# Kernel tuning notes

Hardware: AMD Instinct MI355X
Metric: run time of the kernel (lower is better)

## Reference

```python
import jax, jax.numpy as jnp
import numpy as np

B, T, H = 256, 512, 1024


def setup_inputs() -> dict:
    key = jax.random.key(0)
    ks = jax.random.split(key, 11)
    s = 1.0 / np.sqrt(H)
    u = lambda k, shape: jax.random.uniform(k, shape, jnp.float32, -s, s)
    return {
        "x": jax.random.normal(ks[0], (B, T), jnp.float32),
        "W_ih1": u(ks[1], (4 * H, 1)),
        "W_hh1": u(ks[2], (4 * H, H)),
        "b_ih1": u(ks[3], (4 * H,)),
        "b_hh1": u(ks[4], (4 * H,)),
        "W_ih2": u(ks[5], (4 * H, H)),
        "W_hh2": u(ks[6], (4 * H, H)),
        "b_ih2": u(ks[7], (4 * H,)),
        "b_hh2": u(ks[8], (4 * H,)),
        "W_out": u(ks[9], (1, H)),
        "b_out": u(ks[10], (1,)),
        "future": 0,
    }


def _lstm_cell(x, h, c, W_ih, W_hh, b):
    # PyTorch LSTMCell gate order: i, f, g, o
    gates = x @ W_ih.T + h @ W_hh.T + b
    i, f, g, o = jnp.split(gates, 4, axis=-1)
    c_new = jax.nn.sigmoid(f) * c + jax.nn.sigmoid(i) * jnp.tanh(g)
    h_new = jax.nn.sigmoid(o) * jnp.tanh(c_new)
    return h_new, c_new


def reference(x, W_ih1, W_hh1, b_ih1, b_hh1, W_ih2, W_hh2, b_ih2, b_hh2, W_out, b_out, future):
    Bn = x.shape[0]
    Hd = W_hh1.shape[1]
    b1 = b_ih1 + b_hh1
    b2 = b_ih2 + b_hh2

    def step(carry, x_t):
        h1, c1, h2, c2 = carry
        h1, c1 = _lstm_cell(x_t, h1, c1, W_ih1, W_hh1, b1)
        h2, c2 = _lstm_cell(h1, h2, c2, W_ih2, W_hh2, b2)
        out = h2 @ W_out.T + b_out  # [B, 1]
        return (h1, c1, h2, c2), out

    xs = x.T[:, :, None]  # [T, B, 1]
    carry0 = tuple(jnp.zeros((Bn, Hd), x.dtype) for _ in range(4))
    carry, outs = jax.lax.scan(step, carry0, xs)  # outs: [T, B, 1]
    outputs = [outs[:, :, 0].T]  # [B, T]

    # closed-loop future prediction (future is a static Python int)
    out = outs[-1]
    for _ in range(future):
        carry, out = step(carry, out)
        outputs.append(out)
    return jnp.concatenate(outputs, axis=1)
```

## Files before the change

kernel.cpp:

```cpp
#include <hip/hip_runtime.h>
#include <hip/hip_cooperative_groups.h>
#include <math.h>

namespace cg = cooperative_groups;

#define Bsz 256
#define Tsz 512
#define GSTR 258

using half8 = __attribute__((ext_vector_type(8))) _Float16;
using half4 = __attribute__((ext_vector_type(4))) _Float16;
using f32x4 = __attribute__((ext_vector_type(4))) float;

#define MFMA_V(acc, a, b) (acc) = __builtin_amdgcn_mfma_f32_16x16x32_f16((a), (b), (acc), 0, 0, 0)
#define INV2048 (1.0f / 2048.0f)

__device__ __forceinline__ float sigm(float v)   { return 1.0f / (1.0f + expf(-v)); }
__device__ __forceinline__ float tanh_f(float v) { float e = expf(2.0f * v); return 1.0f - 2.0f / (e + 1.0f); }

__device__ __forceinline__ void split8(const float* p, half8& hi, half8& lo) {
    float4 v0 = *(const float4*)p, v1 = *(const float4*)(p + 4);
    float vv[8] = {v0.x, v0.y, v0.z, v0.w, v1.x, v1.y, v1.z, v1.w};
    #pragma unroll
    for (int j = 0; j < 8; ++j) {
        hi[j] = (_Float16)vv[j];
        lo[j] = (_Float16)((vv[j] - (float)hi[j]) * 2048.0f);
    }
}

__device__ __forceinline__ void st_h4(_Float16* p, half4 v) {
    unsigned long long u;
    __builtin_memcpy(&u, &v, 8);
    __hip_atomic_store((unsigned long long*)(void*)p, u,
                       __ATOMIC_RELAXED, __HIP_MEMORY_SCOPE_AGENT);
}
__device__ __forceinline__ void st_f(float* p, float v) {
    __hip_atomic_store(p, v, __ATOMIC_RELAXED, __HIP_MEMORY_SCOPE_AGENT);
}

__device__ __forceinline__ unsigned ag_add(unsigned* p, unsigned v) {
    return __hip_atomic_fetch_add(p, v, __ATOMIC_RELAXED, __HIP_MEMORY_SCOPE_AGENT);
}
__device__ __forceinline__ unsigned ag_ld(unsigned* p) {
    return __hip_atomic_load(p, __ATOMIC_RELAXED, __HIP_MEMORY_SCOPE_AGENT);
}

__device__ __forceinline__ void busy_fma(float& z) {
    #pragma unroll
    for (int i = 0; i < 16; ++i)
        z = __builtin_fmaf(z, 1.0000001f, 1e-9f);
    asm volatile("" :: "v"(z));
}

__device__ __forceinline__ void step_barrier(unsigned* arrX, unsigned* flagX,
                                             unsigned* bar1, unsigned* dummyv,
                                             unsigned* relFlag,
                                             int isLead, unsigned xcc,
                                             unsigned nLead, unsigned nBlkX,
                                             unsigned it1) {
    __syncthreads();
    if ((threadIdx.x >> 6) == 0) {
        if ((threadIdx.x & 63) == 0) {
            float z = 1.0f;
            ag_add(&arrX[xcc << 5], 1u);
            if (isLead) {
                while (ag_ld(&arrX[xcc << 5]) < nBlkX * it1) busy_fma(z);
                ag_add(bar1, 1u);
                while (ag_ld(bar1) < nLead * it1) busy_fma(z);
                if ((it1 & 3u) == 0u)
                    __hip_atomic_fetch_add(&dummyv[xcc << 5], 1u,
                                           __ATOMIC_ACQ_REL, __HIP_MEMORY_SCOPE_AGENT);
                ag_add(&flagX[xcc << 5], 1u);
            } else {
                while (ag_ld(&flagX[xcc << 5]) < it1) busy_fma(z);
            }
            asm volatile("s_waitcnt vmcnt(0)" ::: "memory");
            __hip_atomic_store(relFlag, it1, __ATOMIC_RELAXED,
                               __HIP_MEMORY_SCOPE_WORKGROUP);
        }
        asm volatile("buffer_inv sc0" ::: "memory");
    } else {
        float z = 1.0f + (float)(threadIdx.x & 63) * 1e-8f;
        while (__hip_atomic_load(relFlag, __ATOMIC_RELAXED,
                                 __HIP_MEMORY_SCOPE_WORKGROUP) < it1)
            busy_fma(z);
        asm volatile("buffer_inv sc0" ::: "memory");
    }
}

__global__ __launch_bounds__(512, 1) void lstm_persist(
    const float* __restrict__ x,
    const float* __restrict__ W_ih1, const float* __restrict__ W_hh1,
    const float* __restrict__ b_ih1, const float* __restrict__ b_hh1,
    const float* __restrict__ W_ih2, const float* __restrict__ W_hh2,
    const float* __restrict__ b_ih2, const float* __restrict__ b_hh2,
    const float* __restrict__ W_out, const float* __restrict__ b_out,
    float* __restrict__ out, char* __restrict__ ws)
{
    __shared__ float gAcc[32 * GSTR];
    __shared__ float poArr[2 * GSTR];
    __shared__ float bp[32], wihp[32], woutp[8];
    __shared__ float bouts_s;
    __shared__ unsigned isLead_s, xcc_s, nLead_s, nBlkX_s;
    __shared__ unsigned relFlag_s;

    cg::grid_group grid = cg::this_grid();

    const int tid  = threadIdx.x;
    const int lane = tid & 63;
    const int wv   = tid >> 6;
    const int m    = lane & 15;
    const int quad = lane >> 4;
    const int bx   = blockIdx.x;
    const bool isL2 = (bx >= 128);
    const int rg   = isL2 ? (bx - 128) : bx;
    const int HO   = rg << 3;

    float*    xT       = (float*)ws;
    _Float16* hswz     = (_Float16*)(ws + (512 << 10));
    float*    partials = (float*)(ws + (512 << 10) + (8 << 20));
    unsigned* bar0     = (unsigned*)(ws + (512 << 10) + (8 << 20) + (512 << 10));
    unsigned* arrX     = bar0 + 512;
    unsigned* flagX    = bar0 + 768;
    unsigned* bar1     = bar0 + 1024;
    unsigned* nLeadCt  = bar0 + 1057;
    unsigned* claimA   = bar0 + 1088;
    unsigned* dummyv   = bar0 + 1536;

    #define HBUF(p, l, hl) (hswz + ((((p) << 2) | ((l) << 1) | (hl)) << 18))

    if (bx == 0)
        for (int i = tid; i < 2048; i += 512) bar0[i] = 0u;
    if (tid < 32) {
        const int row = ((tid & 3) << 10) + HO + (tid >> 2);
        if (!isL2) {
            bp[tid]   = b_ih1[row] + b_hh1[row];
            wihp[tid] = W_ih1[row];
        } else {
            bp[tid] = b_ih2[row] + b_hh2[row];
            if (tid < 8) woutp[tid] = W_out[HO + tid];
        }
        if (tid == 0) { bouts_s = b_out[0]; relFlag_s = 0u; }
    }
    {
        const int gidx = bx * 512 + tid;
        *(float4*)((char*)hswz + (6u << 20) + (size_t)gidx * 16) = make_float4(0, 0, 0, 0);
        xT[gidx] = x[(gidx & 255) * Tsz + (gidx >> 8)];
    }

    grid.sync();

    if (tid == 0) {
        unsigned xcc;
        asm volatile("s_getreg_b32 %0, hwreg(HW_REG_XCC_ID)" : "=s"(xcc));
        xcc &= 7u;
        xcc_s = xcc;
        unsigned old = ag_add(&claimA[xcc << 5], 1u);
        isLead_s = (old == 0u);
        if (old == 0u)
            ag_add(nLeadCt, 1u);
    }
    grid.sync();
    if (tid == 0) {
        nLead_s = ag_ld(nLeadCt);
        nBlkX_s = ag_ld(&claimA[xcc_s << 5]);
    }
    __syncthreads();
    const int      isLead = (int)isLead_s;
    const unsigned xcc    = xcc_s;
    const unsigned nLead  = nLead_s;
    const unsigned nBlkX  = nBlkX_s;

    const int b_ep = tid & 255, hg = tid >> 8;
    const int k0e  = HO + (hg << 2);
    const int wofs = ((b_ep >> 4) << 14) + ((k0e >> 5) << 9)
                   + (((b_ep & 15) | (((k0e >> 3) & 3) << 4)) << 3) + (k0e & 7);

    if (!isL2) {
        half8 wh[2][4], wl[2][4];
        #pragma unroll
        for (int mt = 0; mt < 2; ++mt) {
            const int pr = (mt << 4) + m;
            const size_t rw = (size_t)(((pr & 3) << 10) + HO + (pr >> 2)) << 10;
            #pragma unroll
            for (int kt = 0; kt < 4; ++kt) {
                const int k = (wv << 7) + (kt << 5) + (quad << 3);
                split8(W_hh1 + rw + k, wh[mt][kt], wl[mt][kt]);
            }
        }
        for (int idx = tid; idx < 8192; idx += 512) {
            const int p = idx >> 8, b = idx & 255;
            gAcc[p * GSTR + b] = bp[p] + xT[b] * wihp[p];
        }
        __syncthreads();
        float cr[4] = {0, 0, 0, 0};

        for (int it = 0; it <= Tsz; ++it) {
            const int sW = it & 3;
            const int sR = (it + 3) & 3;
            const int sP = it & 3;

            float xnext = 0.0f;
            if (it + 1 < Tsz) xnext = xT[((it + 1) << 8) + b_ep];

            if (wv == 0 && it >= 2) {
                const float* pp = partials + (sP << 15) + (bx << 7);
                float s = pp[lane] + pp[lane + 64];
                s += __shfl_xor(s, 32); s += __shfl_xor(s, 16); s += __shfl_xor(s, 8);
                s += __shfl_xor(s, 4);  s += __shfl_xor(s, 2);  s += __shfl_xor(s, 1);
                if (lane == 0) st_f(&out[(bx << 9) + (it - 2)], bouts_s + s);
            }

            if (it < Tsz) {
                const _Float16* bhB = HBUF(sR, 0, 0);
                const _Float16* blB = HBUF(sR, 0, 1);
                const int lo_off = (wv << 11) + (lane << 3);
                #pragma unroll 2
                for (int bi = 0; bi < 16; ++bi) {
                    const int btl = (bi + (wv << 1)) & 15;
                    const _Float16* ph = bhB + (btl << 14) + lo_off;
                    const _Float16* pl = blB + (btl << 14) + lo_off;
                    half8 bh[4], bl[4];
                    #pragma unroll
                    for (int kt = 0; kt < 4; ++kt) {
                        bh[kt] = *(const half8*)(ph + (kt << 9));
                        bl[kt] = *(const half8*)(pl + (kt << 9));
                    }
                    f32x4 a0[2] = {(f32x4){0,0,0,0}, (f32x4){0,0,0,0}};
                    f32x4 a1[2] = {(f32x4){0,0,0,0}, (f32x4){0,0,0,0}};
                    #pragma unroll
                    for (int kt = 0; kt < 4; ++kt) {
                        MFMA_V(a0[0], wh[0][kt], bh[kt]);
                        MFMA_V(a1[0], wh[0][kt], bl[kt]);
                        MFMA_V(a1[0], wl[0][kt], bh[kt]);
                        MFMA_V(a0[1], wh[1][kt], bh[kt]);
                        MFMA_V(a1[1], wh[1][kt], bl[kt]);
                        MFMA_V(a1[1], wl[1][kt], bh[kt]);
                    }
                    const int col = (btl << 4) + m;
                    #pragma unroll
                    for (int mt = 0; mt < 2; ++mt)
                        #pragma unroll
                        for (int r = 0; r < 4; ++r)
                            atomicAdd(&gAcc[((mt << 4) + (quad << 2) + r) * GSTR + col],
                                      a0[mt][r] + a1[mt][r] * INV2048);
                }
            }

            __syncthreads();

            if (it < Tsz) {
                half4 hhi, hlo;
                #pragma unroll
                for (int j = 0; j < 4; ++j) {
                    const int p = (hg << 4) + (j << 2);
                    const float gi = gAcc[(p + 0) * GSTR + b_ep];
                    const float gf = gAcc[(p + 1) * GSTR + b_ep];
                    const float gg = gAcc[(p + 2) * GSTR + b_ep];
                    const float go = gAcc[(p + 3) * GSTR + b_ep];
                    const float c  = sigm(gf) * cr[j] + sigm(gi) * tanh_f(gg);
                    cr[j] = c;
                    const float hn = sigm(go) * tanh_f(c);
                    hhi[j] = (_Float16)hn;
                    hlo[j] = (_Float16)((hn - (float)hhi[j]) * 2048.0f);
                }
                st_h4(HBUF(sW, 0, 0) + wofs, hhi);
                st_h4(HBUF(sW, 0, 1) + wofs, hlo);
                if (it + 1 < Tsz) {
                    #pragma unroll
                    for (int p = (hg << 4); p < (hg << 4) + 16; ++p)
                        gAcc[p * GSTR + b_ep] = bp[p] + xnext * wihp[p];
                }
            }

            step_barrier(arrX, flagX, bar1, dummyv, &relFlag_s,
                         isLead, xcc, nLead, nBlkX, (unsigned)(it + 1));
        }
    } else {
        half8 wh[2][8], wl[2][8];
        #pragma unroll
        for (int mt = 0; mt < 2; ++mt) {
            const int pr = (mt << 4) + m;
            const size_t rw = (size_t)(((pr & 3) << 10) + HO + (pr >> 2)) << 10;
            #pragma unroll
            for (int kt = 0; kt < 8; ++kt) {
                const int k = (wv << 8) + (kt << 5) + (quad << 3);
                const float* p = (k < 1024) ? (W_ih2 + rw + k)
                                            : (W_hh2 + rw + k - 1024);
                split8(p, wh[mt][kt], wl[mt][kt]);
            }
        }
        for (int idx = tid; idx < 8192; idx += 512) {
            const int p = idx >> 8, b = idx & 255;
            gAcc[p * GSTR + b] = bp[p];
        }
        __syncthreads();
        float cr[4] = {0, 0, 0, 0};

        for (int it = 0; it <= Tsz; ++it) {
            const int sR1 = (it + 3) & 3;
            const int sW2 = (it + 3) & 3;
            const int sR2 = (it + 2) & 3;
            const int sP  = it & 3;
            const int sPW = (it + 1) & 3;

            if (wv == 0 && it >= 2) {
                const float* pp = partials + (sP << 15) + (bx << 7);
                float s = pp[lane] + pp[lane + 64];
                s += __shfl_xor(s, 32); s += __shfl_xor(s, 16); s += __shfl_xor(s, 8);
                s += __shfl_xor(s, 4);  s += __shfl_xor(s, 2);  s += __shfl_xor(s, 1);
                if (lane == 0) st_f(&out[(bx << 9) + (it - 2)], bouts_s + s);
            }

            if (it >= 1) {
                const bool hi2 = (wv >= 4);
                const _Float16* bhB = hi2 ? HBUF(sR2, 1, 0) : HBUF(sR1, 0, 0);
                const _Float16* blB = hi2 ? HBUF(sR2, 1, 1) : HBUF(sR1, 0, 1);
                const int lo_off = ((wv & 3) << 12) + (lane << 3);
                #pragma unroll 1
                for (int bi = 0; bi < 16; ++bi) {
                    const int btl = (bi + (wv << 1)) & 15;
                    const _Float16* ph = bhB + (btl << 14) + lo_off;
                    const _Float16* pl = blB + (btl << 14) + lo_off;
                    half8 bh[8], bl[8];
                    #pragma unroll
                    for (int kt = 0; kt < 8; ++kt) {
                        bh[kt] = *(const half8*)(ph + (kt << 9));
                        bl[kt] = *(const half8*)(pl + (kt << 9));
                    }
                    f32x4 a0[2] = {(f32x4){0,0,0,0}, (f32x4){0,0,0,0}};
                    f32x4 a1[2] = {(f32x4){0,0,0,0}, (f32x4){0,0,0,0}};
                    #pragma unroll
                    for (int kt = 0; kt < 8; ++kt) {
                        MFMA_V(a0[0], wh[0][kt], bh[kt]);
                        MFMA_V(a1[0], wh[0][kt], bl[kt]);
                        MFMA_V(a1[0], wl[0][kt], bh[kt]);
                        MFMA_V(a0[1], wh[1][kt], bh[kt]);
                        MFMA_V(a1[1], wh[1][kt], bl[kt]);
                        MFMA_V(a1[1], wl[1][kt], bh[kt]);
                    }
                    const int col = (btl << 4) + m;
                    #pragma unroll
                    for (int mt = 0; mt < 2; ++mt)
                        #pragma unroll
                        for (int r = 0; r < 4; ++r)
                            atomicAdd(&gAcc[((mt << 4) + (quad << 2) + r) * GSTR + col],
                                      a0[mt][r] + a1[mt][r] * INV2048);
                }
            }

            __syncthreads();

            if (it >= 1) {
                half4 hhi, hlo;
                float po = 0.0f;
                #pragma unroll
                for (int j = 0; j < 4; ++j) {
                    const int p = (hg << 4) + (j << 2);
                    const float gi = gAcc[(p + 0) * GSTR + b_ep];
                    const float gf = gAcc[(p + 1) * GSTR + b_ep];
                    const float gg = gAcc[(p + 2) * GSTR + b_ep];
                    const float go = gAcc[(p + 3) * GSTR + b_ep];
                    const float c  = sigm(gf) * cr[j] + sigm(gi) * tanh_f(gg);
                    cr[j] = c;
                    const float hn = sigm(go) * tanh_f(c);
                    hhi[j] = (_Float16)hn;
                    hlo[j] = (_Float16)((hn - (float)hhi[j]) * 2048.0f);
                    po += hn * woutp[(hg << 2) + j];
                }
                st_h4(HBUF(sW2, 1, 0) + wofs, hhi);
                st_h4(HBUF(sW2, 1, 1) + wofs, hlo);
                poArr[hg * GSTR + b_ep] = po;
                #pragma unroll
                for (int p = (hg << 4); p < (hg << 4) + 16; ++p)
                    gAcc[p * GSTR + b_ep] = bp[p];
            }
            __syncthreads();
            if (it >= 1 && tid < 256) {
                const float s = poArr[tid] + poArr[GSTR + tid];
                st_f(&partials[(sPW << 15) + (tid << 7) + rg], s);
            }

            step_barrier(arrX, flagX, bar1, dummyv, &relFlag_s,
                         isLead, xcc, nLead, nBlkX, (unsigned)(it + 1));
        }
    }

    if (wv == 0) {
        const float* pp = partials + (1 << 15) + (bx << 7);
        float s = pp[lane] + pp[lane + 64];
        s += __shfl_xor(s, 32); s += __shfl_xor(s, 16); s += __shfl_xor(s, 8);
        s += __shfl_xor(s, 4);  s += __shfl_xor(s, 2);  s += __shfl_xor(s, 1);
        if (lane == 0) st_f(&out[(bx << 9) + (Tsz - 1)], bouts_s + s);
    }
    #undef HBUF
}

extern "C" void kernel_launch(void* const* d_in, const int* in_sizes, int n_in,
                              void* d_out, int out_size, void* d_ws, size_t ws_size,
                              hipStream_t stream)
{
    const float* x     = (const float*)d_in[0];
    const float* W_ih1 = (const float*)d_in[1];
    const float* W_hh1 = (const float*)d_in[2];
    const float* b_ih1 = (const float*)d_in[3];
    const float* b_hh1 = (const float*)d_in[4];
    const float* W_ih2 = (const float*)d_in[5];
    const float* W_hh2 = (const float*)d_in[6];
    const float* b_ih2 = (const float*)d_in[7];
    const float* b_hh2 = (const float*)d_in[8];
    const float* W_out = (const float*)d_in[9];
    const float* b_out = (const float*)d_in[10];
    float* out = (float*)d_out;
    char*  ws  = (char*)d_ws;

    void* args[] = {
        (void*)&x,
        (void*)&W_ih1, (void*)&W_hh1, (void*)&b_ih1, (void*)&b_hh1,
        (void*)&W_ih2, (void*)&W_hh2, (void*)&b_ih2, (void*)&b_hh2,
        (void*)&W_out, (void*)&b_out, (void*)&out, (void*)&ws,
    };
    hipLaunchCooperativeKernel((const void*)lstm_persist,
                               dim3(256), dim3(512), args, 0, stream);
}
```

Measured before the change: 45.92 ms.

## Split layer-2 into separate input-projection and recurrent block groups in a 3-stage pipeline

Layer 2's work, which used a fused K=2048 GEMV in 128 blocks, is now split across two groups of 64 blocks. One group computes W_ih2·h1 and publishes the gate pre-activations through a global double buffer. The other computes W_hh2·h2, adds those buffered values and applies the cell update. Each block covers 16 hidden units instead of 8, and the pipeline depth grows to three stages. This shortens the per-step critical path for layer 2, at the cost of more global traffic, larger register tiles and one extra barrier step.

```diff
diff --git a/kernel.cpp b/kernel.cpp
--- a/kernel.cpp
+++ b/kernel.cpp
@@ -7,6 +7,7 @@
 #define Bsz 256
 #define Tsz 512
 #define GSTR 258
+#define LOOP_END 515
 
 using half8 = __attribute__((ext_vector_type(8))) _Float16;
 using half4 = __attribute__((ext_vector_type(4))) _Float16;
@@ -36,6 +37,9 @@
 }
 __device__ __forceinline__ void st_f(float* p, float v) {
     __hip_atomic_store(p, v, __ATOMIC_RELAXED, __HIP_MEMORY_SCOPE_AGENT);
+}
+__device__ __forceinline__ float agf_ld(const float* p) {
+    return __hip_atomic_load(p, __ATOMIC_RELAXED, __HIP_MEMORY_SCOPE_AGENT);
 }
 
 __device__ __forceinline__ unsigned ag_add(unsigned* p, unsigned v) {
@@ -97,9 +101,8 @@
     const float* __restrict__ W_out, const float* __restrict__ b_out,
     float* __restrict__ out, char* __restrict__ ws)
 {
-    __shared__ float gAcc[32 * GSTR];
-    __shared__ float poArr[2 * GSTR];
-    __shared__ float bp[32], wihp[32], woutp[8];
+    __shared__ float gAcc[64 * GSTR];
+    __shared__ float bp[64], wihp[32], woutp[16];
     __shared__ float bouts_s;
     __shared__ unsigned isLead_s, xcc_s, nLead_s, nBlkX_s;
     __shared__ unsigned relFlag_s;
@@ -112,36 +115,40 @@
     const int m    = lane & 15;
     const int quad = lane >> 4;
     const int bx   = blockIdx.x;
-    const bool isL2 = (bx >= 128);
-    const int rg   = isL2 ? (bx - 128) : bx;
-    const int HO   = rg << 3;
+    const int role = (bx < 128) ? 0 : (bx < 192 ? 1 : 2);
+    const int pa   = bx & 63;
+    const int HO1  = bx << 3;
+    const int HO2  = pa << 4;
 
     float*    xT       = (float*)ws;
     _Float16* hswz     = (_Float16*)(ws + (512 << 10));
     float*    partials = (float*)(ws + (512 << 10) + (8 << 20));
-    unsigned* bar0     = (unsigned*)(ws + (512 << 10) + (8 << 20) + (512 << 10));
+    unsigned* bar0     = (unsigned*)(ws + (9 << 20));
     unsigned* arrX     = bar0 + 512;
     unsigned* flagX    = bar0 + 768;
     unsigned* bar1     = bar0 + 1024;
     unsigned* nLeadCt  = bar0 + 1057;
     unsigned* claimA   = bar0 + 1088;
     unsigned* dummyv   = bar0 + 1536;
+    float*    xbuf     = (float*)(ws + (10 << 20));
 
     #define HBUF(p, l, hl) (hswz + ((((p) << 2) | ((l) << 1) | (hl)) << 18))
 
     if (bx == 0)
         for (int i = tid; i < 2048; i += 512) bar0[i] = 0u;
-    if (tid < 32) {
-        const int row = ((tid & 3) << 10) + HO + (tid >> 2);
-        if (!isL2) {
-            bp[tid]   = b_ih1[row] + b_hh1[row];
-            wihp[tid] = W_ih1[row];
-        } else {
+    if (role == 0 && tid < 32) {
+        const int row = ((tid & 3) << 10) + HO1 + (tid >> 2);
+        bp[tid]   = b_ih1[row] + b_hh1[row];
+        wihp[tid] = W_ih1[row];
+    }
+    if (role == 2) {
+        if (tid < 64) {
+            const int row = ((tid & 3) << 10) + HO2 + (tid >> 2);
             bp[tid] = b_ih2[row] + b_hh2[row];
-            if (tid < 8) woutp[tid] = W_out[HO + tid];
-        }
-        if (tid == 0) { bouts_s = b_out[0]; relFlag_s = 0u; }
-    }
+        }
+        if (tid < 16) woutp[tid] = W_out[HO2 + tid];
+    }
+    if (tid == 0) { bouts_s = b_out[0]; relFlag_s = 0u; }
     {
         const int gidx = bx * 512 + tid;
         *(float4*)((char*)hswz + (6u << 20) + (size_t)gidx * 16) = make_float4(0, 0, 0, 0);
@@ -157,8 +164,7 @@
         xcc_s = xcc;
         unsigned old = ag_add(&claimA[xcc << 5], 1u);
         isLead_s = (old == 0u);
-        if (old == 0u)
-            ag_add(nLeadCt, 1u);
+        if (old == 0u) ag_add(nLeadCt, 1u);
     }
     grid.sync();
     if (tid == 0) {
@@ -172,16 +178,16 @@
     const unsigned nBlkX  = nBlkX_s;
 
     const int b_ep = tid & 255, hg = tid >> 8;
-    const int k0e  = HO + (hg << 2);
-    const int wofs = ((b_ep >> 4) << 14) + ((k0e >> 5) << 9)
-                   + (((b_ep & 15) | (((k0e >> 3) & 3) << 4)) << 3) + (k0e & 7);
-
-    if (!isL2) {
+
+    if (role == 0) {
+        const int k0e  = HO1 + (hg << 2);
+        const int wofs = ((b_ep >> 4) << 14) + ((k0e >> 5) << 9)
+                       + (((b_ep & 15) | (((k0e >> 3) & 3) << 4)) << 3) + (k0e & 7);
         half8 wh[2][4], wl[2][4];
         #pragma unroll
         for (int mt = 0; mt < 2; ++mt) {
             const int pr = (mt << 4) + m;
-            const size_t rw = (size_t)(((pr & 3) << 10) + HO + (pr >> 2)) << 10;
+            const size_t rw = (size_t)(((pr & 3) << 10) + HO1 + (pr >> 2)) << 10;
             #pragma unroll
             for (int kt = 0; kt < 4; ++kt) {
                 const int k = (wv << 7) + (kt << 5) + (quad << 3);
@@ -195,7 +201,7 @@
         __syncthreads();
         float cr[4] = {0, 0, 0, 0};
 
-        for (int it = 0; it <= Tsz; ++it) {
+        for (int it = 0; it < LOOP_END; ++it) {
             const int sW = it & 3;
             const int sR = (it + 3) & 3;
             const int sP = it & 3;
@@ -203,12 +209,12 @@
             float xnext = 0.0f;
             if (it + 1 < Tsz) xnext = xT[((it + 1) << 8) + b_ep];
 
-            if (wv == 0 && it >= 2) {
+            if (wv == 0 && it >= 3) {
                 const float* pp = partials + (sP << 15) + (bx << 7);
                 float s = pp[lane] + pp[lane + 64];
                 s += __shfl_xor(s, 32); s += __shfl_xor(s, 16); s += __shfl_xor(s, 8);
                 s += __shfl_xor(s, 4);  s += __shfl_xor(s, 2);  s += __shfl_xor(s, 1);
-                if (lane == 0) st_f(&out[(bx << 9) + (it - 2)], bouts_s + s);
+                if (lane == 0) st_f(&out[(bx << 9) + (it - 3)], bouts_s + s);
             }
 
             if (it < Tsz) {
@@ -276,72 +282,64 @@
             step_barrier(arrX, flagX, bar1, dummyv, &relFlag_s,
                          isLead, xcc, nLead, nBlkX, (unsigned)(it + 1));
         }
-    } else {
-        half8 wh[2][8], wl[2][8];
+    } else if (role == 1) {
+        half8 wh[4][4], wl[4][4];
         #pragma unroll
-        for (int mt = 0; mt < 2; ++mt) {
+        for (int mt = 0; mt < 4; ++mt) {
             const int pr = (mt << 4) + m;
-            const size_t rw = (size_t)(((pr & 3) << 10) + HO + (pr >> 2)) << 10;
+            const size_t rw = (size_t)(((pr & 3) << 10) + HO2 + (pr >> 2)) << 10;
             #pragma unroll
-            for (int kt = 0; kt < 8; ++kt) {
-                const int k = (wv << 8) + (kt << 5) + (quad << 3);
-                const float* p = (k < 1024) ? (W_ih2 + rw + k)
-                                            : (W_hh2 + rw + k - 1024);
-                split8(p, wh[mt][kt], wl[mt][kt]);
-            }
-        }
-        for (int idx = tid; idx < 8192; idx += 512) {
-            const int p = idx >> 8, b = idx & 255;
-            gAcc[p * GSTR + b] = bp[p];
-        }
+            for (int kt = 0; kt < 4; ++kt) {
+                const int k = (wv << 7) + (kt << 5) + (quad << 3);
+                split8(W_ih2 + rw + k, wh[mt][kt], wl[mt][kt]);
+            }
+        }
+        for (int idx = tid; idx < 16384; idx += 512)
+            gAcc[(idx >> 8) * GSTR + (idx & 255)] = 0.0f;
         __syncthreads();
-        float cr[4] = {0, 0, 0, 0};
-
-        for (int it = 0; it <= Tsz; ++it) {
-            const int sR1 = (it + 3) & 3;
-            const int sW2 = (it + 3) & 3;
-            const int sR2 = (it + 2) & 3;
-            const int sP  = it & 3;
-            const int sPW = (it + 1) & 3;
-
-            if (wv == 0 && it >= 2) {
+
+        for (int it = 0; it < LOOP_END; ++it) {
+            const int S = it;
+            const int sP = it & 3;
+
+            if (wv == 0 && it >= 3) {
                 const float* pp = partials + (sP << 15) + (bx << 7);
                 float s = pp[lane] + pp[lane + 64];
                 s += __shfl_xor(s, 32); s += __shfl_xor(s, 16); s += __shfl_xor(s, 8);
                 s += __shfl_xor(s, 4);  s += __shfl_xor(s, 2);  s += __shfl_xor(s, 1);
-                if (lane == 0) st_f(&out[(bx << 9) + (it - 2)], bouts_s + s);
-            }
-
-            if (it >= 1) {
-                const bool hi2 = (wv >= 4);
-                const _Float16* bhB = hi2 ? HBUF(sR2, 1, 0) : HBUF(sR1, 0, 0);
-                const _Float16* blB = hi2 ? HBUF(sR2, 1, 1) : HBUF(sR1, 0, 1);
-                const int lo_off = ((wv & 3) << 12) + (lane << 3);
+                if (lane == 0) st_f(&out[(bx << 9) + (it - 3)], bouts_s + s);
+            }
+
+            if (S >= 1 && S <= Tsz) {
+                const _Float16* bhB = HBUF((S + 3) & 3, 0, 0);
+                const _Float16* blB = HBUF((S + 3) & 3, 0, 1);
+                const int lo_off = (wv << 11) + (lane << 3);
                 #pragma unroll 1
                 for (int bi = 0; bi < 16; ++bi) {
                     const int btl = (bi + (wv << 1)) & 15;
                     const _Float16* ph = bhB + (btl << 14) + lo_off;
                     const _Float16* pl = blB + (btl << 14) + lo_off;
-                    half8 bh[8], bl[8];
-                    #pragma unroll
-                    for (int kt = 0; kt < 8; ++kt) {
+                    half8 bh[4], bl[4];
+                    #pragma unroll
+                    for (int kt = 0; kt < 4; ++kt) {
                         bh[kt] = *(const half8*)(ph + (kt << 9));
                         bl[kt] = *(const half8*)(pl + (kt << 9));
                     }
-                    f32x4 a0[2] = {(f32x4){0,0,0,0}, (f32x4){0,0,0,0}};
-                    f32x4 a1[2] = {(f32x4){0,0,0,0}, (f32x4){0,0,0,0}};
-                    #pragma unroll
-                    for (int kt = 0; kt < 8; ++kt) {
-                        MFMA_V(a0[0], wh[0][kt], bh[kt]);
-                        MFMA_V(a1[0], wh[0][kt], bl[kt]);
-                        MFMA_V(a1[0], wl[0][kt], bh[kt]);
-                        MFMA_V(a0[1], wh[1][kt], bh[kt]);
-                        MFMA_V(a1[1], wh[1][kt], bl[kt]);
-                        MFMA_V(a1[1], wl[1][kt], bh[kt]);
-                    }
+                    f32x4 a0[4] = {(f32x4){0,0,0,0}, (f32x4){0,0,0,0},
+                                   (f32x4){0,0,0,0}, (f32x4){0,0,0,0}};
+                    f32x4 a1[4] = {(f32x4){0,0,0,0}, (f32x4){0,0,0,0},
+                                   (f32x4){0,0,0,0}, (f32x4){0,0,0,0}};
+                    #pragma unroll
+                    for (int kt = 0; kt < 4; ++kt)
+                        #pragma unroll
+                        for (int mt = 0; mt < 4; ++mt) {
+                            MFMA_V(a0[mt], wh[mt][kt], bh[kt]);
+                            MFMA_V(a1[mt], wh[mt][kt], bl[kt]);
+                            MFMA_V(a1[mt], wl[mt][kt], bh[kt]);
+                        }
                     const int col = (btl << 4) + m;
                     #pragma unroll
-                    for (int mt = 0; mt < 2; ++mt)
+                    for (int mt = 0; mt < 4; ++mt)
                         #pragma unroll
                         for (int r = 0; r < 4; ++r)
                             atomicAdd(&gAcc[((mt << 4) + (quad << 2) + r) * GSTR + col],
@@ -351,47 +349,122 @@
 
             __syncthreads();
 
-            if (it >= 1) {
-                half4 hhi, hlo;
+            if (S >= 1 && S <= Tsz) {
+                float* xb = xbuf + ((size_t)((((S - 1) & 1) << 6) | pa) << 14);
+                for (int idx = tid; idx < 16384; idx += 512) {
+                    const int p = idx >> 8, b = idx & 255;
+                    st_f(&xb[idx], gAcc[p * GSTR + b]);
+                    gAcc[p * GSTR + b] = 0.0f;
+                }
+            }
+
+            step_barrier(arrX, flagX, bar1, dummyv, &relFlag_s,
+                         isLead, xcc, nLead, nBlkX, (unsigned)(it + 1));
+        }
+    } else {
+        const int k0eB  = HO2 + (hg << 3);
+        const int wofsB = ((b_ep >> 4) << 14) + ((k0eB >> 5) << 9)
+                        + (((b_ep & 15) | (((k0eB >> 3) & 3) << 4)) << 3) + (k0eB & 7);
+        half8 wh[4][4], wl[4][4];
+        #pragma unroll
+        for (int mt = 0; mt < 4; ++mt) {
+            const int pr = (mt << 4) + m;
+            const size_t rw = (size_t)(((pr & 3) << 10) + HO2 + (pr >> 2)) << 10;
+            #pragma unroll
+            for (int kt = 0; kt < 4; ++kt) {
+                const int k = (wv << 7) + (kt << 5) + (quad << 3);
+                split8(W_hh2 + rw + k, wh[mt][kt], wl[mt][kt]);
+            }
+        }
+        for (int idx = tid; idx < 16384; idx += 512)
+            gAcc[(idx >> 8) * GSTR + (idx & 255)] = bp[idx >> 8];
+        __syncthreads();
+        float cr[8] = {0, 0, 0, 0, 0, 0, 0, 0};
+
+        for (int it = 0; it < LOOP_END; ++it) {
+            const int S = it;
+            const int sP = it & 3;
+
+            if (wv == 0 && it >= 3) {
+                const float* pp = partials + (sP << 15) + (bx << 7);
+                float s = pp[lane] + pp[lane + 64];
+                s += __shfl_xor(s, 32); s += __shfl_xor(s, 16); s += __shfl_xor(s, 8);
+                s += __shfl_xor(s, 4);  s += __shfl_xor(s, 2);  s += __shfl_xor(s, 1);
+                if (lane == 0) st_f(&out[(bx << 9) + (it - 3)], bouts_s + s);
+            }
+
+            if (S >= 2 && S <= Tsz + 1) {
+                const _Float16* bhB = HBUF((S + 1) & 3, 1, 0);
+                const _Float16* blB = HBUF((S + 1) & 3, 1, 1);
+                const int lo_off = (wv << 11) + (lane << 3);
+                #pragma unroll 1
+                for (int bi = 0; bi < 16; ++bi) {
+                    const int btl = (bi + (wv << 1)) & 15;
+                    const _Float16* ph = bhB + (btl << 14) + lo_off;
+                    const _Float16* pl = blB + (btl << 14) + lo_off;
+                    half8 bh[4], bl[4];
+                    #pragma unroll
+                    for (int kt = 0; kt < 4; ++kt) {
+                        bh[kt] = *(const half8*)(ph + (kt << 9));
+                        bl[kt] = *(const half8*)(pl + (kt << 9));
+                    }
+                    f32x4 a0[4] = {(f32x4){0,0,0,0}, (f32x4){0,0,0,0},
+                                   (f32x4){0,0,0,0}, (f32x4){0,0,0,0}};
+                    f32x4 a1[4] = {(f32x4){0,0,0,0}, (f32x4){0,0,0,0},
+                                   (f32x4){0,0,0,0}, (f32x4){0,0,0,0}};
+                    #pragma unroll
+                    for (int kt = 0; kt < 4; ++kt)
+                        #pragma unroll
+                        for (int mt = 0; mt < 4; ++mt) {
+                            MFMA_V(a0[mt], wh[mt][kt], bh[kt]);
+                            MFMA_V(a1[mt], wh[mt][kt], bl[kt]);
+                            MFMA_V(a1[mt], wl[mt][kt], bh[kt]);
+                        }
+                    const int col = (btl << 4) + m;
+                    #pragma unroll
+                    for (int mt = 0; mt < 4; ++mt)
+                        #pragma unroll
+                        for (int r = 0; r < 4; ++r)
+                            atomicAdd(&gAcc[((mt << 4) + (quad << 2) + r) * GSTR + col],
+                                      a0[mt][r] + a1[mt][r] * INV2048);
+                }
+            }
+
+            __syncthreads();
+
+            if (S >= 2 && S <= Tsz + 1) {
+                const float* xb = xbuf + ((size_t)((((S - 2) & 1) << 6) | pa) << 14);
+                half4 hA, hB, lA, lB;
                 float po = 0.0f;
                 #pragma unroll
-                for (int j = 0; j < 4; ++j) {
-                    const int p = (hg << 4) + (j << 2);
-                    const float gi = gAcc[(p + 0) * GSTR + b_ep];
-                    const float gf = gAcc[(p + 1) * GSTR + b_ep];
-                    const float gg = gAcc[(p + 2) * GSTR + b_ep];
-                    const float go = gAcc[(p + 3) * GSTR + b_ep];
+                for (int j = 0; j < 8; ++j) {
+                    const int p = ((hg << 3) + j) << 2;
+                    const float gi = gAcc[(p + 0) * GSTR + b_ep] + agf_ld(xb + ((p + 0) << 8) + b_ep);
+                    const float gf = gAcc[(p + 1) * GSTR + b_ep] + agf_ld(xb + ((p + 1) << 8) + b_ep);
+                    const float gg = gAcc[(p + 2) * GSTR + b_ep] + agf_ld(xb + ((p + 2) << 8) + b_ep);
+                    const float go = gAcc[(p + 3) * GSTR + b_ep] + agf_ld(xb + ((p + 3) << 8) + b_ep);
                     const float c  = sigm(gf) * cr[j] + sigm(gi) * tanh_f(gg);
                     cr[j] = c;
                     const float hn = sigm(go) * tanh_f(c);
-                    hhi[j] = (_Float16)hn;
-                    hlo[j] = (_Float16)((hn - (float)hhi[j]) * 2048.0f);
-                    po += hn * woutp[(hg << 2) + j];
-                }
-                st_h4(HBUF(sW2, 1, 0) + wofs, hhi);
-                st_h4(HBUF(sW2, 1, 1) + wofs, hlo);
-                poArr[hg * GSTR + b_ep] = po;
+                    const _Float16 hi16 = (_Float16)hn;
+                    const _Float16 lo16 = (_Float16)((hn - (float)hi16) * 2048.0f);
+                    if (j < 4) { hA[j] = hi16; lA[j] = lo16; }
+                    else       { hB[j - 4] = hi16; lB[j - 4] = lo16; }
+                    po += hn * woutp[(hg << 3) + j];
+                }
+                _Float16* dh = HBUF((S + 2) & 3, 1, 0) + wofsB;
+                _Float16* dl = HBUF((S + 2) & 3, 1, 1) + wofsB;
+                st_h4(dh, hA); st_h4(dh + 4, hB);
+                st_h4(dl, lA); st_h4(dl + 4, lB);
+                st_f(&partials[(((S + 1) & 3) << 15) + (b_ep << 7) + (pa << 1) + hg], po);
                 #pragma unroll
-                for (int p = (hg << 4); p < (hg << 4) + 16; ++p)
-                    gAcc[p * GSTR + b_ep] = bp[p];
-            }
-            __syncthreads();
-            if (it >= 1 && tid < 256) {
-                const float s = poArr[tid] + poArr[GSTR + tid];
-                st_f(&partials[(sPW << 15) + (tid << 7) + rg], s);
+                for (int p2 = hg << 5; p2 < (hg << 5) + 32; ++p2)
+                    gAcc[p2 * GSTR + b_ep] = bp[p2];
             }
 
             step_barrier(arrX, flagX, bar1, dummyv, &relFlag_s,
                          isLead, xcc, nLead, nBlkX, (unsigned)(it + 1));
         }
-    }
-
-    if (wv == 0) {
-        const float* pp = partials + (1 << 15) + (bx << 7);
-        float s = pp[lane] + pp[lane + 64];
-        s += __shfl_xor(s, 32); s += __shfl_xor(s, 16); s += __shfl_xor(s, 8);
-        s += __shfl_xor(s, 4);  s += __shfl_xor(s, 2);  s += __shfl_xor(s, 1);
-        if (lane == 0) st_f(&out[(bx << 9) + (Tsz - 1)], bouts_s + s);
     }
     #undef HBUF
 }
```

Result: slower. 93.64 ms (+103.9%).
